# Kernel optimization log

Hardware: AMD Instinct MI355X
Metric: run time of the kernel (lower is better)

The kernel has to match this reference:

```python
import jax, jax.numpy as jnp
import numpy as np

B, D, H, E, K = 8192, 1024, 4096, 8, 2
LOSS_COEF = 0.01
EPS_COMBINE = float(np.finfo(np.float64).eps)  # np.finfo(float).eps used in combine


def setup_inputs() -> dict:
    key = jax.random.key(0)
    ks = jax.random.split(key, 6)
    s_in = 1.0 / np.sqrt(D)
    s_hid = 1.0 / np.sqrt(H)
    return {
        "x": jax.random.normal(ks[0], (B, D), jnp.float32),
        "w_gate": jax.random.uniform(ks[1], (E, D), jnp.float32, -s_in, s_in),
        "fc1_w": jax.random.uniform(ks[2], (E, H, D), jnp.float32, -s_in, s_in),
        "fc1_b": jax.random.uniform(ks[3], (E, H), jnp.float32, -s_in, s_in),
        "fc2_w": jax.random.uniform(ks[4], (E, D, H), jnp.float32, -s_hid, s_hid),
        "fc2_b": jax.random.uniform(ks[5], (E, D), jnp.float32, -s_hid, s_hid),
    }


def _cv_squared(v):
    # torch .var() uses ddof=1
    return jnp.var(v, ddof=1) / (jnp.mean(v) ** 2 + 1e-10)


def _top_k_gating(x, w_gate):
    # clean logits (noisy_gating=False): [B, E]
    logits = x @ w_gate.T
    top_vals, top_idx = jax.lax.top_k(logits, K + 1)  # min(k+1, E)
    topk_vals = top_vals[:, :K]
    topk_idx = top_idx[:, :K]
    topk_gates = jax.nn.softmax(topk_vals, axis=1)
    gates = jnp.zeros((x.shape[0], E), x.dtype)
    gates = gates.at[jnp.arange(x.shape[0])[:, None], topk_idx].set(topk_gates)
    return gates


def _forward(x, w_gate, fc1_w, fc1_b, fc2_w, fc2_b):
    gates = _top_k_gating(x, w_gate)            # [B, E], sparse (k nonzeros/row)
    importance = gates.sum(axis=0)              # [E]
    load = (gates > 0).sum(axis=0).astype(jnp.float32)
    loss = (_cv_squared(importance) + _cv_squared(load)) * LOSS_COEF

    # Dense-equivalent expert compute: tokens with gate==0 contribute 0 to the
    # combine, identical math to SparseDispatcher's gather/scatter.
    h = jnp.einsum('bd,ehd->beh', x, fc1_w) + fc1_b            # [B, E, H]
    h = jax.nn.gelu(h, approximate=False)                      # torch exact gelu
    o = jnp.einsum('beh,edh->bed', h, fc2_w) + fc2_b           # [B, E, D]
    log_p = jax.nn.log_softmax(o, axis=-1)                     # LogSoftmax(dim=1)

    # combine: exp, weight by gates, scatter-add, eps-fill, log
    combined = jnp.einsum('be,bed->bd', gates, jnp.exp(log_p)) # [B, D]
    combined = jnp.where(combined == 0, EPS_COMBINE, combined)
    y = jnp.log(combined)
    return y, loss


def reference(x, w_gate, fc1_w, fc1_b, fc2_w, fc2_b):
    return _forward(x, w_gate, fc1_w, fc1_b, fc2_w, fc2_b)
```

## Files before the change

### kernel.cpp

```cpp
#include <hip/hip_runtime.h>
#include <cstdint>
#include <cmath>

#define BT 8192
#define DD 1024
#define HH 4096
#define EE 8

typedef __attribute__((ext_vector_type(8))) short short8;
typedef __attribute__((ext_vector_type(4))) float f32x4;
typedef unsigned short u16;
typedef unsigned int u32;

__device__ __forceinline__ u16 f2bf(float f) {
    u32 u = __float_as_uint(f);
    u += 0x7FFFu + ((u >> 16) & 1u);
    return (u16)(u >> 16);
}

__device__ __forceinline__ void gld_lds16(const void* g, void* l) {
    __builtin_amdgcn_global_load_lds((__attribute__((address_space(1))) void*)g,
                                     (__attribute__((address_space(3))) void*)l,
                                     16, 0, 0);
}

__global__ void cvt_kernel(const float* __restrict__ src, u16* __restrict__ dst, int n8) {
    int i = blockIdx.x * blockDim.x + threadIdx.x;
    if (i >= n8) return;
    size_t base = (size_t)i * 8;
    float4 a = *(const float4*)(src + base);
    float4 b = *(const float4*)(src + base + 4);
    uint4 o;
    o.x = (u32)f2bf(a.x) | ((u32)f2bf(a.y) << 16);
    o.y = (u32)f2bf(a.z) | ((u32)f2bf(a.w) << 16);
    o.z = (u32)f2bf(b.x) | ((u32)f2bf(b.y) << 16);
    o.w = (u32)f2bf(b.z) | ((u32)f2bf(b.w) << 16);
    *(uint4*)(dst + base) = o;
}

__global__ void gating_kernel(const float* __restrict__ x, const float* __restrict__ wg,
                              float* __restrict__ gate_arr, int* __restrict__ list,
                              int* __restrict__ info,
                              int* __restrict__ counts, float* __restrict__ importance) {
    int wave = (blockIdx.x * blockDim.x + threadIdx.x) >> 6;
    int lane = threadIdx.x & 63;
    if (wave >= BT) return;
    const float* xr = x + (size_t)wave * DD;
    double acc[EE];
#pragma unroll
    for (int e = 0; e < EE; ++e) acc[e] = 0.0;
    for (int i = lane; i < DD; i += 64) {
        double xv = (double)xr[i];
#pragma unroll
        for (int e = 0; e < EE; ++e)
            acc[e] += xv * (double)wg[e * DD + i];
    }
#pragma unroll
    for (int e = 0; e < EE; ++e) {
        double v = acc[e];
        for (int off = 32; off; off >>= 1) v += __shfl_down(v, off, 64);
        acc[e] = v;
    }
    if (lane == 0) {
        int i0 = 0; double v0 = acc[0];
        for (int e = 1; e < EE; ++e) if (acc[e] > v0) { v0 = acc[e]; i0 = e; }
        int i1 = -1; double v1 = -1e300;
        for (int e = 0; e < EE; ++e) { if (e == i0) continue; if (acc[e] > v1) { v1 = acc[e]; i1 = e; } }
        double e1 = exp(v1 - v0);
        double s = 1.0 + e1;
        float g0 = (float)(1.0 / s);
        float g1 = (float)(e1 / s);
        gate_arr[2 * wave]     = g0;
        gate_arr[2 * wave + 1] = g1;
        atomicAdd(&importance[i0], g0);
        atomicAdd(&importance[i1], g1);
        int p0 = atomicAdd(&counts[i0], 1);
        list[i0 * BT + p0] = wave;
        int p1 = atomicAdd(&counts[i1], 1);
        list[i1 * BT + p1] = wave;
        info[2 * wave]     = (i0 << 16) | p0;
        info[2 * wave + 1] = (i1 << 16) | p1;
    }
}

__global__ void loss_kernel(const int* __restrict__ counts, const float* __restrict__ importance,
                            int* __restrict__ offs, float* __restrict__ out_loss) {
    if (threadIdx.x == 0 && blockIdx.x == 0) {
        double mi = 0, ml = 0;
        int off = 0;
        for (int e = 0; e < EE; e++) {
            offs[e] = off; off += counts[e];
            mi += (double)importance[e]; ml += (double)counts[e];
        }
        mi /= EE; ml /= EE;
        double vi = 0, vl = 0;
        for (int e = 0; e < EE; e++) {
            double di = (double)importance[e] - mi; vi += di * di;
            double dl = (double)counts[e] - ml;     vl += dl * dl;
        }
        vi /= (EE - 1); vl /= (EE - 1);
        double cv_i = vi / (mi * mi + 1e-10);
        double cv_l = vl / (ml * ml + 1e-10);
        *out_loss = (float)((cv_i + cv_l) * 0.01);
    }
}

__global__ void gather_x_kernel(const float* __restrict__ x, const int* __restrict__ list,
                                const int* __restrict__ counts, const int* __restrict__ offs,
                                u16* __restrict__ xg) {
    int r = blockIdx.x;
    int e = 0;
#pragma unroll
    for (int i = 1; i < EE; ++i) if (r >= offs[i]) e = i;
    int m = r - offs[e];
    if (m >= counts[e]) return;
    int token = list[e * BT + m];
    const float* src = x + (size_t)token * DD;
    u16* dst = xg + (size_t)r * DD;
    int i = threadIdx.x * 4;
    float4 a = *(const float4*)(src + i);
    uint2 o;
    o.x = (u32)f2bf(a.x) | ((u32)f2bf(a.y) << 16);
    o.y = (u32)f2bf(a.z) | ((u32)f2bf(a.w) << 16);
    *(uint2*)(dst + i) = o;
}

template <int K, int NT, bool GELU, bool GATHER>
__global__ __launch_bounds__(256) void moe_gemm(const u16* __restrict__ Asrc,
                                                const u16* __restrict__ Bsrc,
                                                const float* __restrict__ bias,
                                                const int* __restrict__ list,
                                                const int* __restrict__ counts,
                                                const int* __restrict__ offs,
                                                u16* __restrict__ outB,
                                                float* __restrict__ outF) {
    const int e = blockIdx.z;
    const int cnt = counts[e];
    const int mbase = blockIdx.y * 128;
    if (mbase >= cnt) return;
    const int mmax = cnt - mbase;
    const int rowbase = offs[e] + mbase;
    const int nbase = blockIdx.x * 128;
    const int tid = threadIdx.x;
    const int lane = tid & 63;
    const int wv = tid >> 6;

    __shared__ u16 As[128 * 32];
    __shared__ u16 Bs[128 * 32];
    __shared__ int rows_lds[128];

    if constexpr (GATHER) {
        if (tid < 128) {
            int m = min(tid, mmax - 1);
            rows_lds[tid] = list[e * BT + mbase + m];
        }
        __syncthreads();
    }

    const int myrow = tid & 127;
    const int kch = tid >> 7;
    size_t arow;
    if constexpr (GATHER) arow = (size_t)rows_lds[myrow];
    else                  arow = (size_t)(rowbase + min(myrow, mmax - 1));
    const u16* aptr = Asrc + arow * (size_t)K + kch * 8;
    const u16* bptr = Bsrc + ((size_t)e * NT + nbase + myrow) * (size_t)K + kch * 8;

    f32x4 acc[4][4] = {};
    const int moff = (wv >> 1) * 64;
    const int noff = (wv & 1) * 64;
    const int kq = lane >> 4;
    const int rsub = lane & 15;

    for (int k0 = 0; k0 < K; k0 += 32) {
        gld_lds16(aptr + k0,      &As[tid * 8]);
        gld_lds16(aptr + k0 + 16, &As[(tid + 256) * 8]);
        gld_lds16(bptr + k0,      &Bs[tid * 8]);
        gld_lds16(bptr + k0 + 16, &Bs[(tid + 256) * 8]);
        __syncthreads();
        short8 af[4], bfr[4];
#pragma unroll
        for (int mi = 0; mi < 4; mi++)
            af[mi] = *(const short8*)&As[(kq * 128 + moff + mi * 16 + rsub) * 8];
#pragma unroll
        for (int ni = 0; ni < 4; ni++)
            bfr[ni] = *(const short8*)&Bs[(kq * 128 + noff + ni * 16 + rsub) * 8];
#pragma unroll
        for (int mi = 0; mi < 4; mi++)
#pragma unroll
            for (int ni = 0; ni < 4; ni++)
                acc[mi][ni] = __builtin_amdgcn_mfma_f32_16x16x32_bf16(af[mi], bfr[ni], acc[mi][ni], 0, 0, 0);
        __syncthreads();
    }

    const int rq = (lane >> 4) * 4;
    float bvals[4];
#pragma unroll
    for (int ni = 0; ni < 4; ni++)
        bvals[ni] = bias[(size_t)e * NT + nbase + noff + ni * 16 + rsub];
#pragma unroll
    for (int mi = 0; mi < 4; mi++) {
#pragma unroll
        for (int r = 0; r < 4; r++) {
            int m = moff + mi * 16 + rq + r;
            if (m < mmax) {
                size_t ro = (size_t)(rowbase + m);
#pragma unroll
                for (int ni = 0; ni < 4; ni++) {
                    int n = nbase + noff + ni * 16 + rsub;
                    float v = acc[mi][ni][r] + bvals[ni];
                    if constexpr (GELU) {
                        v = 0.5f * v * (1.0f + erff(v * 0.7071067811865476f));
                        outB[ro * NT + n] = f2bf(v);
                    } else {
                        outF[ro * NT + n] = v;
                    }
                }
            }
        }
    }
}

__global__ void combine_kernel(const float* __restrict__ o, const float* __restrict__ gates,
                               const int* __restrict__ info, const int* __restrict__ offs,
                               float* __restrict__ y) {
    const int b = blockIdx.x;
    const int tid = threadIdx.x;
    const int lane = tid & 63, wv = tid >> 6;
    const int inf0 = info[2 * b], inf1 = info[2 * b + 1];
    const int r0i = offs[inf0 >> 16] + (inf0 & 0xffff);
    const int r1i = offs[inf1 >> 16] + (inf1 & 0xffff);
    const float* r0 = o + (size_t)r0i * DD;
    const float* r1 = o + (size_t)r1i * DD;
    float v0[4], v1[4];
#pragma unroll
    for (int j = 0; j < 4; j++) { v0[j] = r0[tid + 256 * j]; v1[j] = r1[tid + 256 * j]; }
    float m0 = fmaxf(fmaxf(v0[0], v0[1]), fmaxf(v0[2], v0[3]));
    float m1 = fmaxf(fmaxf(v1[0], v1[1]), fmaxf(v1[2], v1[3]));
#pragma unroll
    for (int off = 32; off; off >>= 1) {
        m0 = fmaxf(m0, __shfl_xor(m0, off, 64));
        m1 = fmaxf(m1, __shfl_xor(m1, off, 64));
    }
    __shared__ float sred[2][4];
    if (lane == 0) { sred[0][wv] = m0; sred[1][wv] = m1; }
    __syncthreads();
    m0 = fmaxf(fmaxf(sred[0][0], sred[0][1]), fmaxf(sred[0][2], sred[0][3]));
    m1 = fmaxf(fmaxf(sred[1][0], sred[1][1]), fmaxf(sred[1][2], sred[1][3]));
    float p0[4], p1[4], s0 = 0.f, s1 = 0.f;
#pragma unroll
    for (int j = 0; j < 4; j++) {
        p0[j] = expf(v0[j] - m0); s0 += p0[j];
        p1[j] = expf(v1[j] - m1); s1 += p1[j];
    }
#pragma unroll
    for (int off = 32; off; off >>= 1) {
        s0 += __shfl_xor(s0, off, 64);
        s1 += __shfl_xor(s1, off, 64);
    }
    __shared__ float sred2[2][4];
    if (lane == 0) { sred2[0][wv] = s0; sred2[1][wv] = s1; }
    __syncthreads();
    s0 = sred2[0][0] + sred2[0][1] + sred2[0][2] + sred2[0][3];
    s1 = sred2[1][0] + sred2[1][1] + sred2[1][2] + sred2[1][3];
    const float c0 = gates[2 * b] / s0;
    const float c1 = gates[2 * b + 1] / s1;
#pragma unroll
    for (int j = 0; j < 4; j++) {
        float c = p0[j] * c0 + p1[j] * c1;
        if (c == 0.f) c = 2.2204460492503131e-16f;
        y[(size_t)b * DD + tid + 256 * j] = logf(c);
    }
}

extern "C" void kernel_launch(void* const* d_in, const int* in_sizes, int n_in,
                              void* d_out, int out_size, void* d_ws, size_t ws_size,
                              hipStream_t stream) {
    const float* x     = (const float*)d_in[0];
    const float* wgate = (const float*)d_in[1];
    const float* fc1w  = (const float*)d_in[2];
    const float* fc1b  = (const float*)d_in[3];
    const float* fc2w  = (const float*)d_in[4];
    const float* fc2b  = (const float*)d_in[5];
    float* out = (float*)d_out;

    char* ws = (char*)d_ws;
    const size_t MB = 1024 * 1024;
    const bool big = ws_size >= 289 * MB;
    u16* w1b = (u16*)(ws);
    float* o = (float*)(ws);
    u16* w2b = (u16*)(ws + 64 * MB);
    u16* xb  = (u16*)(ws + 128 * MB);
    u16* h   = (u16*)(ws + (big ? 128 : 144) * MB);
    u16* xg  = (u16*)(ws + 256 * MB);
    char* meta = ws + (big ? 288 : 272) * MB;
    int* counts       = (int*)meta;
    int* offs         = (int*)(meta + 32);
    float* importance = (float*)(meta + 64);
    float* gate_arr   = (float*)(meta + 128);
    int* info         = (int*)(meta + 128 + 65536);
    int* list         = (int*)(meta + 128 + 131072);

    hipMemsetAsync(meta, 0, 96, stream);
    cvt_kernel<<<(EE * HH * DD / 8 + 255) / 256, 256, 0, stream>>>(fc1w, w1b, EE * HH * DD / 8);
    cvt_kernel<<<(EE * DD * HH / 8 + 255) / 256, 256, 0, stream>>>(fc2w, w2b, EE * DD * HH / 8);
    gating_kernel<<<BT / 4, 256, 0, stream>>>(x, wgate, gate_arr, list, info, counts, importance);
    loss_kernel<<<1, 64, 0, stream>>>(counts, importance, offs, out + (size_t)BT * DD);

    if (big) {
        gather_x_kernel<<<2 * BT, 256, 0, stream>>>(x, list, counts, offs, xg);
        moe_gemm<DD, HH, true, false><<<dim3(HH / 128, BT / 128, EE), 256, 0, stream>>>(
            xg, w1b, fc1b, nullptr, counts, offs, h, nullptr);
    } else {
        cvt_kernel<<<(BT * DD / 8 + 255) / 256, 256, 0, stream>>>(x, xb, BT * DD / 8);
        moe_gemm<DD, HH, true, true><<<dim3(HH / 128, BT / 128, EE), 256, 0, stream>>>(
            xb, w1b, fc1b, list, counts, offs, h, nullptr);
    }
    moe_gemm<HH, DD, false, false><<<dim3(DD / 128, BT / 128, EE), 256, 0, stream>>>(
        h, w2b, fc2b, nullptr, counts, offs, nullptr, o);
    combine_kernel<<<BT, 256, 0, stream>>>(o, gate_arr, info, offs, out);
}
```

Baseline: 1.322 ms.

## Compact MoE GEMM grid via tile map, double-buffer LDS, XCD-aware block swizzle

Replaces the 3D grid, which launched many empty blocks for experts with few tokens, with a compact 1D grid. A tile map built in the loss kernel lists only the real (expert, m-tile) pairs, and block ids are remapped so consecutive tiles spread across the 8 XCDs. The K loop now double-buffers the A/B LDS tiles so the next tile's global-to-LDS loads are issued before the current tile's MFMAs. This cuts wasted block launches and some load latency, at the cost of twice the shared memory per block, which may lower occupancy.

```diff
diff --git a/kernel.cpp b/kernel.cpp
--- a/kernel.cpp
+++ b/kernel.cpp
@@ -6,6 +6,7 @@
 #define DD 1024
 #define HH 4096
 #define EE 8
+#define MTMAX 136
 
 typedef __attribute__((ext_vector_type(8))) short short8;
 typedef __attribute__((ext_vector_type(4))) float f32x4;
@@ -84,7 +85,8 @@
 }
 
 __global__ void loss_kernel(const int* __restrict__ counts, const float* __restrict__ importance,
-                            int* __restrict__ offs, float* __restrict__ out_loss) {
+                            int* __restrict__ offs, float* __restrict__ out_loss,
+                            int* __restrict__ tmap, int* __restrict__ ntiles) {
     if (threadIdx.x == 0 && blockIdx.x == 0) {
         double mi = 0, ml = 0;
         int off = 0;
@@ -102,6 +104,11 @@
         double cv_i = vi / (mi * mi + 1e-10);
         double cv_l = vl / (ml * ml + 1e-10);
         *out_loss = (float)((cv_i + cv_l) * 0.01);
+        int ntl = 0;
+        for (int e = 0; e < EE; e++)
+            for (int t = 0; t < counts[e]; t += 128)
+                tmap[ntl++] = (e << 20) | t;
+        *ntiles = ntl;
     }
 }
 
@@ -132,21 +139,31 @@
                                                 const int* __restrict__ list,
                                                 const int* __restrict__ counts,
                                                 const int* __restrict__ offs,
+                                                const int* __restrict__ tmap,
+                                                const int* __restrict__ ntiles,
                                                 u16* __restrict__ outB,
                                                 float* __restrict__ outF) {
-    const int e = blockIdx.z;
+    constexpr int NXT = NT / 128;
+    constexpr int nwg = NXT * MTMAX;
+    constexpr int q = nwg / 8;
+    const int bid = blockIdx.x;
+    const int wg = (bid & 7) * q + (bid >> 3);
+    const int nt = wg / MTMAX;
+    const int mt = wg - nt * MTMAX;
+    if (mt >= *ntiles) return;
+    const int ent = tmap[mt];
+    const int e = ent >> 20;
+    const int mbase = ent & 0xFFFFF;
     const int cnt = counts[e];
-    const int mbase = blockIdx.y * 128;
-    if (mbase >= cnt) return;
     const int mmax = cnt - mbase;
     const int rowbase = offs[e] + mbase;
-    const int nbase = blockIdx.x * 128;
+    const int nbase = nt * 128;
     const int tid = threadIdx.x;
     const int lane = tid & 63;
     const int wv = tid >> 6;
 
-    __shared__ u16 As[128 * 32];
-    __shared__ u16 Bs[128 * 32];
+    __shared__ u16 As0[128 * 32], As1[128 * 32];
+    __shared__ u16 Bs0[128 * 32], Bs1[128 * 32];
     __shared__ int rows_lds[128];
 
     if constexpr (GATHER) {
@@ -171,26 +188,43 @@
     const int kq = lane >> 4;
     const int rsub = lane & 15;
 
-    for (int k0 = 0; k0 < K; k0 += 32) {
-        gld_lds16(aptr + k0,      &As[tid * 8]);
-        gld_lds16(aptr + k0 + 16, &As[(tid + 256) * 8]);
-        gld_lds16(bptr + k0,      &Bs[tid * 8]);
-        gld_lds16(bptr + k0 + 16, &Bs[(tid + 256) * 8]);
+#define STAGE(Ad, Bd, k0)                                        \
+    do {                                                         \
+        gld_lds16(aptr + (k0),      &(Ad)[tid * 8]);             \
+        gld_lds16(aptr + (k0) + 16, &(Ad)[(tid + 256) * 8]);     \
+        gld_lds16(bptr + (k0),      &(Bd)[tid * 8]);             \
+        gld_lds16(bptr + (k0) + 16, &(Bd)[(tid + 256) * 8]);     \
+    } while (0)
+
+#define COMPUTE(Ad, Bd)                                                              \
+    do {                                                                             \
+        short8 af[4], bfr[4];                                                        \
+        _Pragma("unroll")                                                            \
+        for (int mi = 0; mi < 4; mi++)                                               \
+            af[mi] = *(const short8*)&(Ad)[(kq * 128 + moff + mi * 16 + rsub) * 8];  \
+        _Pragma("unroll")                                                            \
+        for (int ni = 0; ni < 4; ni++)                                               \
+            bfr[ni] = *(const short8*)&(Bd)[(kq * 128 + noff + ni * 16 + rsub) * 8]; \
+        _Pragma("unroll")                                                            \
+        for (int mi = 0; mi < 4; mi++)                                               \
+            _Pragma("unroll")                                                        \
+            for (int ni = 0; ni < 4; ni++)                                           \
+                acc[mi][ni] = __builtin_amdgcn_mfma_f32_16x16x32_bf16(                \
+                    af[mi], bfr[ni], acc[mi][ni], 0, 0, 0);                          \
+    } while (0)
+
+    STAGE(As0, Bs0, 0);
+    __syncthreads();
+    for (int k0 = 0; k0 < K; k0 += 64) {
+        STAGE(As1, Bs1, k0 + 32);
+        COMPUTE(As0, Bs0);
         __syncthreads();
-        short8 af[4], bfr[4];
-#pragma unroll
-        for (int mi = 0; mi < 4; mi++)
-            af[mi] = *(const short8*)&As[(kq * 128 + moff + mi * 16 + rsub) * 8];
-#pragma unroll
-        for (int ni = 0; ni < 4; ni++)
-            bfr[ni] = *(const short8*)&Bs[(kq * 128 + noff + ni * 16 + rsub) * 8];
-#pragma unroll
-        for (int mi = 0; mi < 4; mi++)
-#pragma unroll
-            for (int ni = 0; ni < 4; ni++)
-                acc[mi][ni] = __builtin_amdgcn_mfma_f32_16x16x32_bf16(af[mi], bfr[ni], acc[mi][ni], 0, 0, 0);
+        if (k0 + 64 < K) STAGE(As0, Bs0, k0 + 64);
+        COMPUTE(As1, Bs1);
         __syncthreads();
     }
+#undef STAGE
+#undef COMPUTE
 
     const int rq = (lane >> 4) * 4;
     float bvals[4];
@@ -296,26 +330,28 @@
     int* counts       = (int*)meta;
     int* offs         = (int*)(meta + 32);
     float* importance = (float*)(meta + 64);
+    int* ntiles       = (int*)(meta + 96);
     float* gate_arr   = (float*)(meta + 128);
     int* info         = (int*)(meta + 128 + 65536);
     int* list         = (int*)(meta + 128 + 131072);
+    int* tmap         = (int*)(meta + 512 * 1024);
 
     hipMemsetAsync(meta, 0, 96, stream);
     cvt_kernel<<<(EE * HH * DD / 8 + 255) / 256, 256, 0, stream>>>(fc1w, w1b, EE * HH * DD / 8);
     cvt_kernel<<<(EE * DD * HH / 8 + 255) / 256, 256, 0, stream>>>(fc2w, w2b, EE * DD * HH / 8);
     gating_kernel<<<BT / 4, 256, 0, stream>>>(x, wgate, gate_arr, list, info, counts, importance);
-    loss_kernel<<<1, 64, 0, stream>>>(counts, importance, offs, out + (size_t)BT * DD);
+    loss_kernel<<<1, 64, 0, stream>>>(counts, importance, offs, out + (size_t)BT * DD, tmap, ntiles);
 
     if (big) {
         gather_x_kernel<<<2 * BT, 256, 0, stream>>>(x, list, counts, offs, xg);
-        moe_gemm<DD, HH, true, false><<<dim3(HH / 128, BT / 128, EE), 256, 0, stream>>>(
-            xg, w1b, fc1b, nullptr, counts, offs, h, nullptr);
+        moe_gemm<DD, HH, true, false><<<(HH / 128) * MTMAX, 256, 0, stream>>>(
+            xg, w1b, fc1b, nullptr, counts, offs, tmap, ntiles, h, nullptr);
     } else {
         cvt_kernel<<<(BT * DD / 8 + 255) / 256, 256, 0, stream>>>(x, xb, BT * DD / 8);
-        moe_gemm<DD, HH, true, true><<<dim3(HH / 128, BT / 128, EE), 256, 0, stream>>>(
-            xb, w1b, fc1b, list, counts, offs, h, nullptr);
-    }
-    moe_gemm<HH, DD, false, false><<<dim3(DD / 128, BT / 128, EE), 256, 0, stream>>>(
-        h, w2b, fc2b, nullptr, counts, offs, nullptr, o);
+        moe_gemm<DD, HH, true, true><<<(HH / 128) * MTMAX, 256, 0, stream>>>(
+            xb, w1b, fc1b, list, counts, offs, tmap, ntiles, h, nullptr);
+    }
+    moe_gemm<HH, DD, false, false><<<(DD / 128) * MTMAX, 256, 0, stream>>>(
+        h, w2b, fc2b, nullptr, counts, offs, tmap, ntiles, nullptr, o);
     combine_kernel<<<BT, 256, 0, stream>>>(o, gate_arr, info, offs, out);
 }
```

After: 1.320 ms. No clear change (-0.2%).
